# Kernel tuning notes

Hardware: AMD Instinct MI355X
Metric: run time of the kernel (lower is better)

Reference implementation:

```python
import jax, jax.numpy as jnp
import numpy as np

NEG_INF = -9e15
ALPHA = 0.2  # LeakyReLU negative slope


def setup_inputs() -> dict:
    key = jax.random.key(0)
    k1, k2, k3, k4 = jax.random.split(key, 4)
    B, N, C_IN, C_OUT, H = 8, 2048, 256, 256, 4
    node_feats = jax.random.normal(k1, (B, N, C_IN), dtype=jnp.float32)
    adj_matrix = jax.random.randint(k2, (B, N, N), 0, 2, dtype=jnp.int32)
    # include self-connections as the docstring expects
    eye = jnp.eye(N, dtype=jnp.int32)[None]
    adj_matrix = jnp.maximum(adj_matrix, eye)
    W = jax.random.normal(k3, (C_OUT, C_IN), dtype=jnp.float32) * (1.414 / np.sqrt(C_IN))
    b = jnp.zeros((C_OUT,), dtype=jnp.float32)
    a = jax.random.normal(k4, (H, 2 * (C_OUT // H)), dtype=jnp.float32) * 0.1
    return {"node_feats": node_feats, "adj_matrix": adj_matrix, "W": W, "b": b, "a": a}


def reference(node_feats, adj_matrix, W, b, a):
    B, N, _ = node_feats.shape
    H, two_c = a.shape
    c = two_c // 2
    # projection: [B, N, H, c]
    f = (jnp.einsum('bni,oi->bno', node_feats, W) + b).reshape(B, N, H, c)
    # attention logit for edge (i, j): leakyrelu(a . [f_i, f_j])
    # decomposes as leakyrelu(s_src[i] + s_dst[j])
    a_src, a_dst = a[:, :c], a[:, c:]
    s_src = jnp.einsum('bnhc,hc->bnh', f, a_src)  # [B, N, H]
    s_dst = jnp.einsum('bnhc,hc->bnh', f, a_dst)  # [B, N, H]
    logits = jax.nn.leaky_relu(s_src[:, :, None, :] + s_dst[:, None, :, :], ALPHA)  # [B,N,N,H]
    logits = jnp.where(adj_matrix[..., None] == 1, logits, NEG_INF)
    probs = jax.nn.softmax(logits, axis=2)  # softmax over source nodes j
    out = jnp.einsum('bijh,bjhc->bihc', probs, f)
    return out.reshape(B, N, H * c)  # concat_heads=True
```

## Files before the change

### kernel.cpp

```cpp
#include <hip/hip_runtime.h>

#define LOG2E 1.4426950408889634f

typedef __attribute__((ext_vector_type(8))) short short8;
typedef __attribute__((ext_vector_type(16))) float f32x16;

__device__ __forceinline__ unsigned short f2bf(float f) {
  unsigned int u = __float_as_uint(f);
  u = (u + 0x7fffu + ((u >> 16) & 1u)) >> 16;
  return (unsigned short)u;
}

__global__ __launch_bounds__(256) void gat_k1(
    const float* __restrict__ X, const float* __restrict__ W,
    const float* __restrict__ bias, const float* __restrict__ a,
    unsigned short* __restrict__ ft, float* __restrict__ ssrc,
    float* __restrict__ sdst)
{
  __shared__ float Xs[8][128];
  __shared__ float Ws[8][128];
  const int tid = threadIdx.x;
  const int tx = tid & 15, ty = tid >> 4;
  const int m0 = blockIdx.x * 128;
  const int c0 = blockIdx.y * 128;

  float acc[8][8];
#pragma unroll
  for (int r = 0; r < 8; ++r)
#pragma unroll
    for (int j = 0; j < 8; ++j) acc[r][j] = 0.f;

  const int lrow = tid >> 1;
  const int kk0 = (tid & 1) * 4;
  const float* Xp = X + (size_t)(m0 + lrow) * 256 + kk0;
  const float* Wp = W + (size_t)(c0 + lrow) * 256 + kk0;

  for (int kc = 0; kc < 256; kc += 8) {
    float4 xv = *(const float4*)(Xp + kc);
    float4 wv = *(const float4*)(Wp + kc);
    __syncthreads();
    Xs[kk0 + 0][lrow] = xv.x; Xs[kk0 + 1][lrow] = xv.y;
    Xs[kk0 + 2][lrow] = xv.z; Xs[kk0 + 3][lrow] = xv.w;
    Ws[kk0 + 0][lrow] = wv.x; Ws[kk0 + 1][lrow] = wv.y;
    Ws[kk0 + 2][lrow] = wv.z; Ws[kk0 + 3][lrow] = wv.w;
    __syncthreads();
#pragma unroll
    for (int kk = 0; kk < 8; ++kk) {
      float av[8], wv8[8];
#pragma unroll
      for (int r = 0; r < 8; ++r) av[r] = Xs[kk][ty * 8 + r];
#pragma unroll
      for (int j = 0; j < 8; ++j) wv8[j] = Ws[kk][tx * 8 + j];
#pragma unroll
      for (int r = 0; r < 8; ++r)
#pragma unroll
        for (int j = 0; j < 8; ++j) acc[r][j] = fmaf(av[r], wv8[j], acc[r][j]);
    }
  }

  const int b = m0 >> 11;
  const int nloc0 = (m0 & 2047) + ty * 8;
  const int cg0 = c0 + tx * 8;
  const int h = cg0 >> 6;
  const int cb = cg0 & 63;

  float bv[8], av_s[8], av_d[8];
#pragma unroll
  for (int j = 0; j < 8; ++j) {
    bv[j]   = bias[cg0 + j];
    av_s[j] = a[h * 128 + cb + j];
    av_d[j] = a[h * 128 + 64 + cb + j];
  }
#pragma unroll
  for (int r = 0; r < 8; ++r)
#pragma unroll
    for (int j = 0; j < 8; ++j) acc[r][j] += bv[j];

  const int jt = nloc0 >> 4;
  const int ni = nloc0 & 15;
#pragma unroll
  for (int j = 0; j < 8; ++j) {
    unsigned int u[4];
#pragma unroll
    for (int q = 0; q < 4; ++q) {
      unsigned int lo = f2bf(acc[2 * q + 0][j]);
      unsigned int hi = f2bf(acc[2 * q + 1][j]);
      u[q] = lo | (hi << 16);
    }
    size_t off = ((((size_t)b * 128 + jt) * 4 + h) * 64 + (cb + j)) * 16 + ni;
    *(uint4*)(ft + off) = make_uint4(u[0], u[1], u[2], u[3]);
  }

  float sp[8], dp[8];
#pragma unroll
  for (int r = 0; r < 8; ++r) {
    float s = 0.f, d = 0.f;
#pragma unroll
    for (int j = 0; j < 8; ++j) {
      s = fmaf(acc[r][j], av_s[j], s);
      d = fmaf(acc[r][j], av_d[j], d);
    }
    sp[r] = s; dp[r] = d;
  }
#pragma unroll
  for (int off = 1; off < 8; off <<= 1) {
#pragma unroll
    for (int r = 0; r < 8; ++r) {
      sp[r] += __shfl_xor(sp[r], off);
      dp[r] += __shfl_xor(dp[r], off);
    }
  }
  if ((tx & 7) == 0) {
    float* sb = ssrc + ((size_t)b * 4 + h) * 2048 + nloc0;
    float* db = sdst + ((size_t)b * 4 + h) * 2048 + nloc0;
#pragma unroll
    for (int r = 0; r < 8; ++r) { sb[r] = sp[r] * LOG2E; db[r] = dp[r] * LOG2E; }
  }
}

#define FT_PITCH 72
#define FT_BYTES (256 * FT_PITCH)
#define ADJ_PITCH 40
#define ADJ_BYTES (32 * ADJ_PITCH)

__global__ __launch_bounds__(512, 4) void gat_k2(
    const int* __restrict__ adj, const unsigned short* __restrict__ ft,
    const float* __restrict__ ssrc, const float* __restrict__ sdst,
    float* __restrict__ out)
{
  __shared__ __align__(16) unsigned char lds[2 * FT_BYTES + 2 * ADJ_BYTES];
  unsigned char* ftile = lds;
  unsigned char* adjb  = lds + 2 * FT_BYTES;

  const int tid = threadIdx.x;
  const int b = blockIdx.x & 7;
  const int itile = blockIdx.x >> 3;
  const int i0 = itile * 32;
  const int w = tid >> 6;
  const int h = w >> 1;
  const int p = w & 1;
  const int lane = tid & 63;
  const int l31 = lane & 31;
  const int kh = lane >> 5;

  const float si = ssrc[((size_t)b * 4 + h) * 2048 + i0 + l31];
  const float* sdh = sdst + ((size_t)b * 4 + h) * 2048;
  const size_t adjbase = (size_t)b * 2048 * 2048 + (size_t)i0 * 2048;

  auto wft = [&](unsigned char* base, int idx, uint4 v) {
    const int half = idx & 1, row = (idx >> 1) & 255, q2 = idx >> 9;
    unsigned char* d = base + row * FT_PITCH + q2 * 32 + half * 16;
    *(uint2*)d       = make_uint2(v.x, v.y);
    *(uint2*)(d + 8) = make_uint2(v.z, v.w);
  };
  const int arow = tid >> 4, aj = (tid & 15) * 2;

  {
    const uint4* src = (const uint4*)(ft + ((size_t)b * 128) * 4096);
    uint4 f0 = src[tid], f1 = src[tid + 512];
    int2 av = *(const int2*)(adj + adjbase + (size_t)arow * 2048 + aj);
    wft(ftile, tid, f0);
    wft(ftile, tid + 512, f1);
    unsigned short pk = (unsigned short)((av.x ? 1u : 0u) | (av.y ? 0x100u : 0u));
    *(unsigned short*)(adjb + arow * ADJ_PITCH + aj) = pk;
  }

  f32x16 acc0, acc1;
#pragma unroll
  for (int q = 0; q < 16; ++q) { acc0[q] = 0.f; acc1[q] = 0.f; }
  float lsum = 0.f;

  __syncthreads();

  for (int s = 0; s < 64; ++s) {
    const int cur = s & 1;
    const int sn = (s < 63) ? s + 1 : 63;
    const uint4* src = (const uint4*)(ft + ((size_t)b * 128 + (size_t)sn * 2) * 4096);
    uint4 f0 = src[tid], f1 = src[tid + 512];
    int2 av = *(const int2*)(adj + adjbase + (size_t)arow * 2048 + sn * 32 + aj);

    const unsigned char* fb  = ftile + cur * FT_BYTES;
    const unsigned char* ab_ = adjb + cur * ADJ_BYTES;
    const int jloc = p * 16 + kh * 8;
    const int j0 = s * 32;

    uint2 am = *(const uint2*)(ab_ + l31 * ADJ_PITCH + jloc);
    const float* tp = sdh + j0 + jloc;
    float4 t0 = *(const float4*)tp;
    float4 t1 = *(const float4*)(tp + 4);
    float tj[8] = {t0.x, t0.y, t0.z, t0.w, t1.x, t1.y, t1.z, t1.w};

    float e[8];
#pragma unroll
    for (int q = 0; q < 8; ++q) {
      float x = si + tj[q];
      float y = fmaxf(x, 0.2f * x);
      float ev = __builtin_amdgcn_exp2f(y);
      unsigned byte = (q < 4) ? ((am.x >> (8 * q)) & 0xffu)
                              : ((am.y >> (8 * (q - 4))) & 0xffu);
      ev = byte ? ev : 0.f;
      e[q] = ev;
      lsum += ev;
    }
    union { unsigned u[4]; short8 v; } af;
#pragma unroll
    for (int q2 = 0; q2 < 4; ++q2) {
      unsigned r;
      asm("v_cvt_pk_bf16_f32 %0, %1, %2" : "=v"(r) : "v"(e[2 * q2]), "v"(e[2 * q2 + 1]));
      af.u[q2] = r;
    }

    const unsigned char* r0 = fb + (h * 64 + l31) * FT_PITCH + jloc * 2;
    const unsigned char* r1 = fb + (h * 64 + l31 + 32) * FT_PITCH + jloc * 2;
    union { unsigned u[4]; short8 v; } b0, b1;
    uint2 x0 = *(const uint2*)r0, x1 = *(const uint2*)(r0 + 8);
    uint2 y0 = *(const uint2*)r1, y1 = *(const uint2*)(r1 + 8);
    b0.u[0] = x0.x; b0.u[1] = x0.y; b0.u[2] = x1.x; b0.u[3] = x1.y;
    b1.u[0] = y0.x; b1.u[1] = y0.y; b1.u[2] = y1.x; b1.u[3] = y1.y;

    acc0 = __builtin_amdgcn_mfma_f32_32x32x16_bf16(af.v, b0.v, acc0, 0, 0, 0);
    acc1 = __builtin_amdgcn_mfma_f32_32x32x16_bf16(af.v, b1.v, acc1, 0, 0, 0);

    if (s < 63) {
      unsigned char* fdst = ftile + (cur ^ 1) * FT_BYTES;
      wft(fdst, tid, f0);
      wft(fdst, tid + 512, f1);
      unsigned short pk = (unsigned short)((av.x ? 1u : 0u) | (av.y ? 0x100u : 0u));
      *(unsigned short*)(adjb + (cur ^ 1) * ADJ_BYTES + arow * ADJ_PITCH + aj) = pk;
    }
    __syncthreads();
  }

  float lsum2 = lsum + __shfl_xor(lsum, 32);
  float* ep = (float*)lds;
  float* el = (float*)(lds + 32768);
  if (p == 1) {
#pragma unroll
    for (int reg = 0; reg < 16; ++reg) {
      const int row = (reg & 3) + 8 * (reg >> 2) + 4 * kh;
      ep[(h * 32 + row) * 64 + l31]      = acc0[reg];
      ep[(h * 32 + row) * 64 + l31 + 32] = acc1[reg];
    }
    if (lane < 32) el[h * 32 + l31] = lsum2;
  }
  __syncthreads();
  if (p == 0) {
    const float L = lsum2 + el[h * 32 + l31];
    const float rinv = 1.0f / L;
    float* ob = out + ((size_t)(b * 2048 + i0)) * 256 + h * 64;
#pragma unroll
    for (int reg = 0; reg < 16; ++reg) {
      const int row = (reg & 3) + 8 * (reg >> 2) + 4 * kh;
      const float ri = __shfl(rinv, row);
      const float o0 = (acc0[reg] + ep[(h * 32 + row) * 64 + l31]) * ri;
      const float o1 = (acc1[reg] + ep[(h * 32 + row) * 64 + l31 + 32]) * ri;
      ob[(size_t)row * 256 + l31]      = o0;
      ob[(size_t)row * 256 + l31 + 32] = o1;
    }
  }
}

extern "C" void kernel_launch(void* const* d_in, const int* in_sizes, int n_in,
                              void* d_out, int out_size, void* d_ws, size_t ws_size,
                              hipStream_t stream) {
  const float* X    = (const float*)d_in[0];
  const int*   adj  = (const int*)d_in[1];
  const float* W    = (const float*)d_in[2];
  const float* bias = (const float*)d_in[3];
  const float* a    = (const float*)d_in[4];
  float* out = (float*)d_out;

  unsigned short* ft = (unsigned short*)d_ws;
  float* ssrc = (float*)((char*)d_ws + 8388608);
  float* sdst = ssrc + 8 * 4 * 2048;

  gat_k1<<<dim3(128, 2, 1), 256, 0, stream>>>(X, W, bias, a, ft, ssrc, sdst);
  gat_k2<<<dim3(512, 1, 1), 512, 0, stream>>>(adj, ft, ssrc, sdst, out);
}
```

Baseline: 111.0 us.

## Load MFMA operands and adjacency directly from global with register double-buffering

The main loop no longer stages feature tiles and packed adjacency in shared memory with a __syncthreads every step. Each lane now loads its MFMA B fragments and adjacency ints straight from global into registers, double-buffered across iterations. The s_dst scores for the batch go into LDS once at kernel start. This drops the per-iteration barrier and the LDS round-trip, but it depends on ft already being in the matching fragment layout. It also gives up coalescing, since each lane reads 32 bytes of adjacency per row with no reuse across waves, and register pressure rises.

```diff
diff --git a/kernel.cpp b/kernel.cpp
--- a/kernel.cpp
+++ b/kernel.cpp
@@ -118,19 +118,13 @@
   }
 }
 
-#define FT_PITCH 72
-#define FT_BYTES (256 * FT_PITCH)
-#define ADJ_PITCH 40
-#define ADJ_BYTES (32 * ADJ_PITCH)
-
 __global__ __launch_bounds__(512, 4) void gat_k2(
     const int* __restrict__ adj, const unsigned short* __restrict__ ft,
     const float* __restrict__ ssrc, const float* __restrict__ sdst,
     float* __restrict__ out)
 {
-  __shared__ __align__(16) unsigned char lds[2 * FT_BYTES + 2 * ADJ_BYTES];
-  unsigned char* ftile = lds;
-  unsigned char* adjb  = lds + 2 * FT_BYTES;
+  __shared__ __align__(16) unsigned char lds[33280];
+  float* sd = (float*)lds;
 
   const int tid = threadIdx.x;
   const int b = blockIdx.x & 7;
@@ -143,27 +137,19 @@
   const int l31 = lane & 31;
   const int kh = lane >> 5;
 
+  {
+    const float4* src = (const float4*)(sdst + (size_t)b * 4 * 2048);
+    float4* dst = (float4*)sd;
+#pragma unroll
+    for (int q = 0; q < 4; ++q) dst[tid + q * 512] = src[tid + q * 512];
+  }
   const float si = ssrc[((size_t)b * 4 + h) * 2048 + i0 + l31];
-  const float* sdh = sdst + ((size_t)b * 4 + h) * 2048;
-  const size_t adjbase = (size_t)b * 2048 * 2048 + (size_t)i0 * 2048;
-
-  auto wft = [&](unsigned char* base, int idx, uint4 v) {
-    const int half = idx & 1, row = (idx >> 1) & 255, q2 = idx >> 9;
-    unsigned char* d = base + row * FT_PITCH + q2 * 32 + half * 16;
-    *(uint2*)d       = make_uint2(v.x, v.y);
-    *(uint2*)(d + 8) = make_uint2(v.z, v.w);
-  };
-  const int arow = tid >> 4, aj = (tid & 15) * 2;
-
-  {
-    const uint4* src = (const uint4*)(ft + ((size_t)b * 128) * 4096);
-    uint4 f0 = src[tid], f1 = src[tid + 512];
-    int2 av = *(const int2*)(adj + adjbase + (size_t)arow * 2048 + aj);
-    wft(ftile, tid, f0);
-    wft(ftile, tid + 512, f1);
-    unsigned short pk = (unsigned short)((av.x ? 1u : 0u) | (av.y ? 0x100u : 0u));
-    *(unsigned short*)(adjb + arow * ADJ_PITCH + aj) = pk;
-  }
+
+  const unsigned short* ftb =
+      ft + ((((size_t)b * 128 + p) * 4 + h) * 64 + l31) * 16 + kh * 8;
+  const int* adjp = adj + (size_t)b * 2048 * 2048 +
+                    (size_t)(i0 + l31) * 2048 + p * 16 + kh * 8;
+  const float* sdh = sd + h * 2048 + p * 16 + kh * 8;
 
   f32x16 acc0, acc1;
 #pragma unroll
@@ -172,33 +158,30 @@
 
   __syncthreads();
 
-  for (int s = 0; s < 64; ++s) {
-    const int cur = s & 1;
-    const int sn = (s < 63) ? s + 1 : 63;
-    const uint4* src = (const uint4*)(ft + ((size_t)b * 128 + (size_t)sn * 2) * 4096);
-    uint4 f0 = src[tid], f1 = src[tid + 512];
-    int2 av = *(const int2*)(adj + adjbase + (size_t)arow * 2048 + sn * 32 + aj);
-
-    const unsigned char* fb  = ftile + cur * FT_BYTES;
-    const unsigned char* ab_ = adjb + cur * ADJ_BYTES;
-    const int jloc = p * 16 + kh * 8;
-    const int j0 = s * 32;
-
-    uint2 am = *(const uint2*)(ab_ + l31 * ADJ_PITCH + jloc);
-    const float* tp = sdh + j0 + jloc;
+  struct Pref { uint4 fb0, fb1; int4 a0, a1; };
+
+  auto LOADS = [&](int s, Pref& P) {
+    const unsigned short* fp = ftb + (size_t)s * 8192;
+    P.fb0 = *(const uint4*)fp;
+    P.fb1 = *(const uint4*)(fp + 512);
+    const int* ap = adjp + s * 32;
+    P.a0 = *(const int4*)ap;
+    P.a1 = *(const int4*)(ap + 4);
+  };
+
+  auto COMP = [&](int s, const Pref& P) {
+    const float* tp = sdh + s * 32;
     float4 t0 = *(const float4*)tp;
     float4 t1 = *(const float4*)(tp + 4);
     float tj[8] = {t0.x, t0.y, t0.z, t0.w, t1.x, t1.y, t1.z, t1.w};
-
+    int ai[8] = {P.a0.x, P.a0.y, P.a0.z, P.a0.w, P.a1.x, P.a1.y, P.a1.z, P.a1.w};
     float e[8];
 #pragma unroll
     for (int q = 0; q < 8; ++q) {
       float x = si + tj[q];
       float y = fmaxf(x, 0.2f * x);
       float ev = __builtin_amdgcn_exp2f(y);
-      unsigned byte = (q < 4) ? ((am.x >> (8 * q)) & 0xffu)
-                              : ((am.y >> (8 * (q - 4))) & 0xffu);
-      ev = byte ? ev : 0.f;
+      ev = ai[q] ? ev : 0.f;
       e[q] = ev;
       lsum += ev;
     }
@@ -209,31 +192,28 @@
       asm("v_cvt_pk_bf16_f32 %0, %1, %2" : "=v"(r) : "v"(e[2 * q2]), "v"(e[2 * q2 + 1]));
       af.u[q2] = r;
     }
-
-    const unsigned char* r0 = fb + (h * 64 + l31) * FT_PITCH + jloc * 2;
-    const unsigned char* r1 = fb + (h * 64 + l31 + 32) * FT_PITCH + jloc * 2;
-    union { unsigned u[4]; short8 v; } b0, b1;
-    uint2 x0 = *(const uint2*)r0, x1 = *(const uint2*)(r0 + 8);
-    uint2 y0 = *(const uint2*)r1, y1 = *(const uint2*)(r1 + 8);
-    b0.u[0] = x0.x; b0.u[1] = x0.y; b0.u[2] = x1.x; b0.u[3] = x1.y;
-    b1.u[0] = y0.x; b1.u[1] = y0.y; b1.u[2] = y1.x; b1.u[3] = y1.y;
-
+    union { uint4 q; short8 v; } b0, b1;
+    b0.q = P.fb0; b1.q = P.fb1;
     acc0 = __builtin_amdgcn_mfma_f32_32x32x16_bf16(af.v, b0.v, acc0, 0, 0, 0);
     acc1 = __builtin_amdgcn_mfma_f32_32x32x16_bf16(af.v, b1.v, acc1, 0, 0, 0);
-
-    if (s < 63) {
-      unsigned char* fdst = ftile + (cur ^ 1) * FT_BYTES;
-      wft(fdst, tid, f0);
-      wft(fdst, tid + 512, f1);
-      unsigned short pk = (unsigned short)((av.x ? 1u : 0u) | (av.y ? 0x100u : 0u));
-      *(unsigned short*)(adjb + (cur ^ 1) * ADJ_BYTES + arow * ADJ_PITCH + aj) = pk;
-    }
-    __syncthreads();
-  }
+  };
+
+  Pref A, B;
+  LOADS(0, A);
+  for (int s = 0; s < 62; s += 2) {
+    LOADS(s + 1, B);
+    COMP(s, A);
+    LOADS(s + 2, A);
+    COMP(s + 1, B);
+  }
+  LOADS(63, B);
+  COMP(62, A);
+  COMP(63, B);
 
   float lsum2 = lsum + __shfl_xor(lsum, 32);
   float* ep = (float*)lds;
   float* el = (float*)(lds + 32768);
+  __syncthreads();
   if (p == 1) {
 #pragma unroll
     for (int reg = 0; reg < 16; ++reg) {
```

Result: slower. 125.4 us (+12.9%).
